# Kernel optimization log

Measured on AMD Instinct MI355X. Metric: run time of the kernel, lower is better.

Reference implementation:

```python
import jax, jax.numpy as jnp
import numpy as np

TWO_PI = 2.0 * np.pi
LN_EPS = 1e-5


def _periods(out_dim, nb):
    # periods[i,j,g] = i*(out_dim*nb) + j*nb + g + 2
    return jnp.arange(out_dim * out_dim * nb, dtype=jnp.float32).reshape(out_dim, out_dim, nb) + 2.0


def _layer(x, M, gamma, beta, P, residual):
    # x: (B,S,in), M: (out,in), P: (out,out,nb)
    out_dim, _, nb = P.shape
    S = x.shape[1]
    xt = jnp.matmul(x, M.T)  # (B,S,out)
    mu = jnp.mean(xt, axis=-1, keepdims=True)
    var = jnp.mean((xt - mu) ** 2, axis=-1, keepdims=True)
    xn = (xt - mu) / jnp.sqrt(var + LN_EPS) * gamma + beta
    pos = jnp.arange(S, dtype=jnp.float32)[:, None, None, None]  # (S,1,1,1)
    phi = jnp.cos(TWO_PI * pos / _periods(out_dim, nb)[None])  # (S,out,out,nb)
    W = jnp.einsum('ijg,sijg->sij', P, phi)  # (S,out,out) contract basis first
    Nk = jnp.einsum('bsj,sij->bsi', xn, W)  # (B,S,out)
    return Nk + residual


def setup_inputs() -> dict:
    key = jax.random.key(0)
    ks = jax.random.split(key, 8)
    B, S, D_in, D, NB = 8, 1024, 64, 96, 8
    u = lambda k, shape, a: jax.random.uniform(k, shape, jnp.float32, -a, a)
    return {
        'seq': jax.random.normal(ks[0], (B, S, D_in), jnp.float32),
        'M1': u(ks[1], (D, D_in), 0.5),
        'P1': u(ks[2], (D, D, NB), 0.1),
        'Wres1': u(ks[3], (D, D_in), 0.1),
        'g1': jnp.ones((D,), jnp.float32),
        'b1': jnp.zeros((D,), jnp.float32),
        'M2': u(ks[4], (D, D), 0.5),
        'P2': u(ks[5], (D, D, NB), 0.1),
        'g2': jnp.ones((D,), jnp.float32),
        'b2': jnp.zeros((D,), jnp.float32),
    }


def reference(seq, M1, P1, Wres1, g1, b1, M2, P2, g2, b2):
    # Layer 1: 64 -> 96, 'separate' residual uses a Linear projection
    x1 = _layer(seq, M1, g1, b1, P1, jnp.matmul(seq, Wres1.T))
    # Layer 2: 96 -> 96, 'separate' residual with in_dim==out_dim is Identity
    x2 = _layer(x1, M2, g2, b2, P2, x1)
    return x2
```

## Files before the change

kernel.cpp:

```cpp
#include <hip/hip_runtime.h>

#define S_LEN    1024
#define B_SZ     8
#define D_IN     64
#define D_OUT    96
#define NB       8
#define SPAD     100
#define WPAD     100
#define NTHREADS 256

__device__ __forceinline__ void compute_W(float* __restrict__ w,
                                          const float* __restrict__ P,
                                          int s, int tid) {
    const float sf = (float)s;
    for (int e = tid; e < D_OUT * D_OUT; e += NTHREADS) {
        float pl[8];
        *(float4*)(&pl[0]) = *(const float4*)(P + e * NB);
        *(float4*)(&pl[4]) = *(const float4*)(P + e * NB + 4);
        float acc = 0.0f;
        const int base = e * NB + 2;
        if (e < 128) {
            #pragma unroll
            for (int g = 0; g < NB; ++g) {
                int per = base + g;
                int r = (s >= per) ? (s % per) : s;
                float v = (float)r * __builtin_amdgcn_rcpf((float)per);
                v -= floorf(v);
                acc = fmaf(pl[g], __builtin_amdgcn_cosf(v), acc);
            }
        } else {
            #pragma unroll
            for (int g = 0; g < NB; ++g) {
                int per = base + g;
                float v = sf * __builtin_amdgcn_rcpf((float)per);
                v -= floorf(v);
                acc = fmaf(pl[g], __builtin_amdgcn_cosf(v), acc);
            }
        }
        int i = e / D_OUT;
        w[e + (WPAD - D_OUT) * i] = acc;
    }
}

__device__ __forceinline__ void block_layernorm(float* __restrict__ buf,
                                                const float* __restrict__ gamma,
                                                const float* __restrict__ beta,
                                                int tid) {
    const int b = tid >> 5;
    const int r = tid & 31;
    float* row = buf + b * SPAD;
    float v0 = row[r], v1 = row[r + 32], v2 = row[r + 64];
    float sum = v0 + v1 + v2;
    float sq  = fmaf(v0, v0, fmaf(v1, v1, v2 * v2));
    #pragma unroll
    for (int off = 16; off > 0; off >>= 1) {
        sum += __shfl_down(sum, off, 32);
        sq  += __shfl_down(sq,  off, 32);
    }
    sum = __shfl(sum, 0, 32);
    sq  = __shfl(sq,  0, 32);
    const float mu  = sum * (1.0f / 96.0f);
    const float var = fmaf(sq, 1.0f / 96.0f, -(mu * mu));
    const float rs  = rsqrtf(var + 1e-5f);
    row[r]      = fmaf((v0 - mu) * rs, gamma[r],      beta[r]);
    row[r + 32] = fmaf((v1 - mu) * rs, gamma[r + 32], beta[r + 32]);
    row[r + 64] = fmaf((v2 - mu) * rs, gamma[r + 64], beta[r + 64]);
}

__global__ void __launch_bounds__(NTHREADS)
hier_fused(const float* __restrict__ seq,  const float* __restrict__ M1,
           const float* __restrict__ P1,   const float* __restrict__ Wres1,
           const float* __restrict__ g1,   const float* __restrict__ b1,
           const float* __restrict__ M2,   const float* __restrict__ P2,
           const float* __restrict__ g2,   const float* __restrict__ b2,
           float* __restrict__ out) {
    __shared__ __align__(16) float w[D_OUT * WPAD];
    __shared__ __align__(16) float xin[B_SZ * SPAD];
    __shared__ __align__(16) float xn[B_SZ * SPAD];
    __shared__ __align__(16) float x1b[B_SZ * SPAD];

    const int s   = blockIdx.x;
    const int tid = threadIdx.x;

    for (int idx = tid; idx < B_SZ * D_IN; idx += NTHREADS) {
        int b = idx >> 6, k = idx & (D_IN - 1);
        xin[b * SPAD + k] = seq[(b * S_LEN + s) * D_IN + k];
    }
    compute_W(w, P1, s, tid);
    __syncthreads();

    for (int idx = tid; idx < B_SZ * D_OUT; idx += NTHREADS) {
        int i = idx >> 3, b = idx & 7;
        const float4* m  = (const float4*)(M1 + i * D_IN);
        const float4* wr = (const float4*)(Wres1 + i * D_IN);
        const float*  xr = xin + b * SPAD;
        float at = 0.0f, ar = 0.0f;
        #pragma unroll
        for (int k = 0; k < D_IN / 4; ++k) {
            float4 mv = m[k], rv = wr[k];
            float x0 = xr[4*k], x1 = xr[4*k+1], x2 = xr[4*k+2], x3 = xr[4*k+3];
            at = fmaf(mv.x, x0, fmaf(mv.y, x1, fmaf(mv.z, x2, fmaf(mv.w, x3, at))));
            ar = fmaf(rv.x, x0, fmaf(rv.y, x1, fmaf(rv.z, x2, fmaf(rv.w, x3, ar))));
        }
        xn[b * SPAD + i]  = at;
        x1b[b * SPAD + i] = ar;
    }
    __syncthreads();

    block_layernorm(xn, g1, b1, tid);
    __syncthreads();

    for (int idx = tid; idx < B_SZ * D_OUT; idx += NTHREADS) {
        int i = idx >> 3, b = idx & 7;
        const float* wrow = w + i * WPAD;
        const float* xr   = xn + b * SPAD;
        float acc = 0.0f;
        #pragma unroll
        for (int j = 0; j < D_OUT / 4; ++j) {
            float4 wv = *(const float4*)(wrow + 4 * j);
            float4 xv = *(const float4*)(xr + 4 * j);
            acc = fmaf(wv.x, xv.x, fmaf(wv.y, xv.y, fmaf(wv.z, xv.z, fmaf(wv.w, xv.w, acc))));
        }
        x1b[b * SPAD + i] += acc;
    }
    __syncthreads();

    compute_W(w, P2, s, tid);

    for (int idx = tid; idx < B_SZ * D_OUT; idx += NTHREADS) {
        int i = idx >> 3, b = idx & 7;
        const float4* m  = (const float4*)(M2 + i * D_OUT);
        const float*  xr = x1b + b * SPAD;
        float at = 0.0f;
        #pragma unroll
        for (int k = 0; k < D_OUT / 4; ++k) {
            float4 mv = m[k];
            at = fmaf(mv.x, xr[4*k], fmaf(mv.y, xr[4*k+1],
                 fmaf(mv.z, xr[4*k+2], fmaf(mv.w, xr[4*k+3], at))));
        }
        xn[b * SPAD + i] = at;
    }
    __syncthreads();

    block_layernorm(xn, g2, b2, tid);
    __syncthreads();

    for (int idx = tid; idx < B_SZ * D_OUT; idx += NTHREADS) {
        int i = idx >> 3, b = idx & 7;
        const float* wrow = w + i * WPAD;
        const float* xr   = xn + b * SPAD;
        float acc = 0.0f;
        #pragma unroll
        for (int j = 0; j < D_OUT / 4; ++j) {
            float4 wv = *(const float4*)(wrow + 4 * j);
            float4 xv = *(const float4*)(xr + 4 * j);
            acc = fmaf(wv.x, xv.x, fmaf(wv.y, xv.y, fmaf(wv.z, xv.z, fmaf(wv.w, xv.w, acc))));
        }
        out[(b * S_LEN + s) * D_OUT + i] = acc + x1b[b * SPAD + i];
    }
}

extern "C" void kernel_launch(void* const* d_in, const int* in_sizes, int n_in,
                              void* d_out, int out_size, void* d_ws, size_t ws_size,
                              hipStream_t stream) {
    const float* seq   = (const float*)d_in[0];
    const float* M1    = (const float*)d_in[1];
    const float* P1    = (const float*)d_in[2];
    const float* Wres1 = (const float*)d_in[3];
    const float* g1    = (const float*)d_in[4];
    const float* b1    = (const float*)d_in[5];
    const float* M2    = (const float*)d_in[6];
    const float* P2    = (const float*)d_in[7];
    const float* g2    = (const float*)d_in[8];
    const float* b2    = (const float*)d_in[9];
    float* out = (float*)d_out;

    hier_fused<<<dim3(S_LEN), dim3(NTHREADS), 0, stream>>>(
        seq, M1, P1, Wres1, g1, b1, M2, P2, g2, b2, out);
}
```

Measured before the change: 147.0 us.

## Share cosine basis across both layers, keep W2 in registers, store W as half

Computes the cosine basis once per element and uses it for both layers' position-dependent weight matrices. The layer-2 weights are held in registers until needed, which removes the second basis pass. Both weight matrices are stored in shared memory as fp16, halving LDS footprint so launch bounds can request 4 blocks per CU. The exact-modulo path for small periods is dropped and weights lose precision to fp16, which risks accuracy, and holding 36 weights per thread raises register pressure.

```diff
diff --git a/kernel.cpp b/kernel.cpp
--- a/kernel.cpp
+++ b/kernel.cpp
@@ -1,4 +1,5 @@
 #include <hip/hip_runtime.h>
+#include <hip/hip_fp16.h>
 
 #define S_LEN    1024
 #define B_SZ     8
@@ -6,41 +7,9 @@
 #define D_OUT    96
 #define NB       8
 #define SPAD     100
-#define WPAD     100
+#define HPAD     104
 #define NTHREADS 256
-
-__device__ __forceinline__ void compute_W(float* __restrict__ w,
-                                          const float* __restrict__ P,
-                                          int s, int tid) {
-    const float sf = (float)s;
-    for (int e = tid; e < D_OUT * D_OUT; e += NTHREADS) {
-        float pl[8];
-        *(float4*)(&pl[0]) = *(const float4*)(P + e * NB);
-        *(float4*)(&pl[4]) = *(const float4*)(P + e * NB + 4);
-        float acc = 0.0f;
-        const int base = e * NB + 2;
-        if (e < 128) {
-            #pragma unroll
-            for (int g = 0; g < NB; ++g) {
-                int per = base + g;
-                int r = (s >= per) ? (s % per) : s;
-                float v = (float)r * __builtin_amdgcn_rcpf((float)per);
-                v -= floorf(v);
-                acc = fmaf(pl[g], __builtin_amdgcn_cosf(v), acc);
-            }
-        } else {
-            #pragma unroll
-            for (int g = 0; g < NB; ++g) {
-                int per = base + g;
-                float v = sf * __builtin_amdgcn_rcpf((float)per);
-                v -= floorf(v);
-                acc = fmaf(pl[g], __builtin_amdgcn_cosf(v), acc);
-            }
-        }
-        int i = e / D_OUT;
-        w[e + (WPAD - D_OUT) * i] = acc;
-    }
-}
+#define EPT      36
 
 __device__ __forceinline__ void block_layernorm(float* __restrict__ buf,
                                                 const float* __restrict__ gamma,
@@ -67,26 +36,71 @@
     row[r + 64] = fmaf((v2 - mu) * rs, gamma[r + 64], beta[r + 64]);
 }
 
-__global__ void __launch_bounds__(NTHREADS)
+__device__ __forceinline__ float nk_dot(const __half* __restrict__ wrow,
+                                        const float* __restrict__ xr) {
+    float acc = 0.0f;
+    #pragma unroll
+    for (int j = 0; j < D_OUT / 8; ++j) {
+        float4 raw = *(const float4*)(wrow + 8 * j);
+        const __half2* hp = (const __half2*)&raw;
+        float2 c0 = __half22float2(hp[0]);
+        float2 c1 = __half22float2(hp[1]);
+        float2 c2 = __half22float2(hp[2]);
+        float2 c3 = __half22float2(hp[3]);
+        float4 xv0 = *(const float4*)(xr + 8 * j);
+        float4 xv1 = *(const float4*)(xr + 8 * j + 4);
+        acc = fmaf(c0.x, xv0.x, acc); acc = fmaf(c0.y, xv0.y, acc);
+        acc = fmaf(c1.x, xv0.z, acc); acc = fmaf(c1.y, xv0.w, acc);
+        acc = fmaf(c2.x, xv1.x, acc); acc = fmaf(c2.y, xv1.y, acc);
+        acc = fmaf(c3.x, xv1.z, acc); acc = fmaf(c3.y, xv1.w, acc);
+    }
+    return acc;
+}
+
+__global__ void __launch_bounds__(NTHREADS, 4)
 hier_fused(const float* __restrict__ seq,  const float* __restrict__ M1,
            const float* __restrict__ P1,   const float* __restrict__ Wres1,
            const float* __restrict__ g1,   const float* __restrict__ b1,
            const float* __restrict__ M2,   const float* __restrict__ P2,
            const float* __restrict__ g2,   const float* __restrict__ b2,
            float* __restrict__ out) {
-    __shared__ __align__(16) float w[D_OUT * WPAD];
+    __shared__ __align__(16) __half wh[D_OUT * HPAD];
     __shared__ __align__(16) float xin[B_SZ * SPAD];
-    __shared__ __align__(16) float xn[B_SZ * SPAD];
+    __shared__ __align__(16) float xn [B_SZ * SPAD];
     __shared__ __align__(16) float x1b[B_SZ * SPAD];
 
     const int s   = blockIdx.x;
     const int tid = threadIdx.x;
+    const float sf = (float)s;
 
     for (int idx = tid; idx < B_SZ * D_IN; idx += NTHREADS) {
         int b = idx >> 6, k = idx & (D_IN - 1);
         xin[b * SPAD + k] = seq[(b * S_LEN + s) * D_IN + k];
     }
-    compute_W(w, P1, s, tid);
+
+    float w2r[EPT];
+    #pragma unroll
+    for (int it = 0; it < EPT; ++it) {
+        const int e = tid + it * NTHREADS;
+        float p1l[8], p2l[8];
+        *(float4*)(&p1l[0]) = *(const float4*)(P1 + e * NB);
+        *(float4*)(&p1l[4]) = *(const float4*)(P1 + e * NB + 4);
+        *(float4*)(&p2l[0]) = *(const float4*)(P2 + e * NB);
+        *(float4*)(&p2l[4]) = *(const float4*)(P2 + e * NB + 4);
+        float a1 = 0.0f, a2 = 0.0f;
+        #pragma unroll
+        for (int g = 0; g < NB; ++g) {
+            float pf = (float)(e * NB + 2 + g);
+            float v  = sf * __builtin_amdgcn_rcpf(pf);
+            v -= floorf(v);
+            float c = __builtin_amdgcn_cosf(v);
+            a1 = fmaf(p1l[g], c, a1);
+            a2 = fmaf(p2l[g], c, a2);
+        }
+        const int i = e / D_OUT, j = e - i * D_OUT;
+        wh[i * HPAD + j] = __float2half(a1);
+        w2r[it] = a2;
+    }
     __syncthreads();
 
     for (int idx = tid; idx < B_SZ * D_OUT; idx += NTHREADS) {
@@ -102,7 +116,7 @@
             at = fmaf(mv.x, x0, fmaf(mv.y, x1, fmaf(mv.z, x2, fmaf(mv.w, x3, at))));
             ar = fmaf(rv.x, x0, fmaf(rv.y, x1, fmaf(rv.z, x2, fmaf(rv.w, x3, ar))));
         }
-        xn[b * SPAD + i]  = at;
+        xn [b * SPAD + i] = at;
         x1b[b * SPAD + i] = ar;
     }
     __syncthreads();
@@ -112,20 +126,16 @@
 
     for (int idx = tid; idx < B_SZ * D_OUT; idx += NTHREADS) {
         int i = idx >> 3, b = idx & 7;
-        const float* wrow = w + i * WPAD;
-        const float* xr   = xn + b * SPAD;
-        float acc = 0.0f;
-        #pragma unroll
-        for (int j = 0; j < D_OUT / 4; ++j) {
-            float4 wv = *(const float4*)(wrow + 4 * j);
-            float4 xv = *(const float4*)(xr + 4 * j);
-            acc = fmaf(wv.x, xv.x, fmaf(wv.y, xv.y, fmaf(wv.z, xv.z, fmaf(wv.w, xv.w, acc))));
-        }
-        x1b[b * SPAD + i] += acc;
+        x1b[b * SPAD + i] += nk_dot(wh + i * HPAD, xn + b * SPAD);
     }
     __syncthreads();
 
-    compute_W(w, P2, s, tid);
+    #pragma unroll
+    for (int it = 0; it < EPT; ++it) {
+        const int e = tid + it * NTHREADS;
+        const int i = e / D_OUT, j = e - i * D_OUT;
+        wh[i * HPAD + j] = __float2half(w2r[it]);
+    }
 
     for (int idx = tid; idx < B_SZ * D_OUT; idx += NTHREADS) {
         int i = idx >> 3, b = idx & 7;
@@ -147,15 +157,7 @@
 
     for (int idx = tid; idx < B_SZ * D_OUT; idx += NTHREADS) {
         int i = idx >> 3, b = idx & 7;
-        const float* wrow = w + i * WPAD;
-        const float* xr   = xn + b * SPAD;
-        float acc = 0.0f;
-        #pragma unroll
-        for (int j = 0; j < D_OUT / 4; ++j) {
-            float4 wv = *(const float4*)(wrow + 4 * j);
-            float4 xv = *(const float4*)(xr + 4 * j);
-            acc = fmaf(wv.x, xv.x, fmaf(wv.y, xv.y, fmaf(wv.z, xv.z, fmaf(wv.w, xv.w, acc))));
-        }
+        float acc = nk_dot(wh + i * HPAD, xn + b * SPAD);
         out[(b * S_LEN + s) * D_OUT + i] = acc + x1b[b * SPAD + i];
     }
 }
```

Result: slower. 247.1 us (+68.1%).
